# Optimization experiments

Hardware: AMD Instinct MI355X
Metric: run time of the kernel (lower is better)

Reference implementation:

```python
import jax, jax.numpy as jnp
import numpy as np

DIM = 1024
HEADS = 16
DIM_HEAD = 64
INNER = HEADS * DIM_HEAD
SCALE = DIM_HEAD ** -0.5


def rotate_half(t):
    # '... (j d) -> ... j d' with j=2: split last dim in half
    x1, x2 = jnp.split(t, 2, axis=-1)
    return jnp.concatenate((-x2, x1), axis=-1)


def rotary_pos(n, d, dtype):
    inv_freq = 1.0 / (10000.0 ** (jnp.arange(0, d, 2, dtype=jnp.float32) / d))
    freqs = jnp.arange(n, dtype=jnp.float32)[:, None] * inv_freq[None, :]  # (n, d/2)
    return jnp.concatenate((freqs, freqs), axis=-1).astype(dtype)  # (n, d)


def apply_rope(pos, t):
    return t * jnp.cos(pos) + rotate_half(t) * jnp.sin(pos)


def setup_inputs() -> dict:
    key = jax.random.key(0)
    ks = jax.random.split(key, 5)
    x = jax.random.normal(ks[0], (2, 2048, DIM), dtype=jnp.float32)
    gamma = jnp.ones((DIM,), dtype=jnp.float32)
    beta = jnp.zeros((DIM,), dtype=jnp.float32)
    Wq = jax.random.normal(ks[1], (DIM, INNER), dtype=jnp.float32) * 0.02
    Wkv = jax.random.normal(ks[2], (DIM, 2 * INNER), dtype=jnp.float32) * 0.02
    Wo = jax.random.normal(ks[3], (INNER, DIM), dtype=jnp.float32) * 0.02
    return {"x": x, "gamma": gamma, "beta": beta, "Wq": Wq, "Wkv": Wkv, "Wo": Wo}


def reference(x, gamma, beta, Wq, Wkv, Wo):
    b, n, _ = x.shape
    # LayerNorm with learned gamma, fixed-zero beta buffer
    mu = jnp.mean(x, axis=-1, keepdims=True)
    var = jnp.var(x, axis=-1, keepdims=True)
    xn = (x - mu) / jnp.sqrt(var + 1e-5) * gamma + beta

    q = xn @ Wq                       # (b, n, inner)
    kv = xn @ Wkv
    k, v = jnp.split(kv, 2, axis=-1)

    def to_heads(t):
        return t.reshape(b, n, HEADS, DIM_HEAD).transpose(0, 2, 1, 3)  # b h n d

    q, k, v = map(to_heads, (q, k, v))

    pos = rotary_pos(n, DIM_HEAD, x.dtype)  # (n, d)
    q = apply_rope(pos, q)
    k = apply_rope(pos, k)

    q = q * SCALE
    sim = jnp.einsum('bhid,bhjd->bhij', q, k)

    neg = -jnp.finfo(sim.dtype).max
    causal_mask = jnp.triu(jnp.ones((n, n), dtype=bool), k=1)
    sim = jnp.where(causal_mask, neg, sim)

    attn = jax.nn.softmax(sim, axis=-1)
    out = jnp.einsum('bhij,bhjd->bhid', attn, v)
    out = out.transpose(0, 2, 1, 3).reshape(b, n, INNER)
    return out @ Wo
```

## Files before the change

kernel.cpp:

```cpp
#include <hip/hip_runtime.h>
#include <stdint.h>

typedef unsigned short u16;
typedef __attribute__((ext_vector_type(8))) short short8;
typedef __attribute__((ext_vector_type(4))) float floatx4;
typedef __attribute__((ext_vector_type(4))) unsigned short u16x4;
typedef __attribute__((ext_vector_type(2))) unsigned int uint2v;

__device__ __forceinline__ float bf2f(u16 v) {
  union { uint32_t u; float f; } x; x.u = ((uint32_t)v) << 16; return x.f;
}
__device__ __forceinline__ u16 f2bf(float f) {
  union { float f; uint32_t u; } x; x.f = f;
  uint32_t r = x.u + 0x7fffu + ((x.u >> 16) & 1u);
  return (u16)(r >> 16);
}
__device__ __forceinline__ uint32_t fu(float f) {
  union { float f; uint32_t u; } x; x.f = f; return x.u;
}

#define GL2LDS(g, l)                                                          \
  __builtin_amdgcn_global_load_lds(                                           \
      (const __attribute__((address_space(1))) void*)(g),                     \
      (__attribute__((address_space(3))) void*)(l), 16, 0, 0)

#define WAITBAR(N)                                                            \
  asm volatile("s_waitcnt vmcnt(" #N ")\n\ts_barrier" ::: "memory")

__global__ __launch_bounds__(256) void prep_k(const float* __restrict__ x,
                                              const float* __restrict__ gamma,
                                              const float* __restrict__ beta,
                                              const float* __restrict__ Wq,
                                              const float* __restrict__ Wkv,
                                              const float* __restrict__ Wo,
                                              u16* __restrict__ xn,
                                              u16* __restrict__ wqkvT,
                                              u16* __restrict__ woT) {
  int bid = blockIdx.x;
  int t = threadIdx.x;
  if (bid < 4096) {
    int row = bid;
    const float* xr = x + (size_t)row * 1024;
    float4 xv = *(const float4*)(xr + t * 4);
    float v0 = xv.x, v1 = xv.y, v2 = xv.z, v3 = xv.w;
    float s = v0 + v1 + v2 + v3;
    float s2 = v0 * v0 + v1 * v1 + v2 * v2 + v3 * v3;
#pragma unroll
    for (int d = 1; d < 64; d <<= 1) {
      s += __shfl_xor(s, d, 64);
      s2 += __shfl_xor(s2, d, 64);
    }
    __shared__ float red[8];
    int lane = t & 63, wv = t >> 6;
    if (lane == 0) { red[wv] = s; red[4 + wv] = s2; }
    __syncthreads();
    s = red[0] + red[1] + red[2] + red[3];
    s2 = red[4] + red[5] + red[6] + red[7];
    float mu = s * (1.0f / 1024.0f);
    float var = s2 * (1.0f / 1024.0f) - mu * mu;
    float rstd = rsqrtf(var + 1e-5f);
    float4 gv = *(const float4*)(gamma + t * 4);
    float4 bv = *(const float4*)(beta + t * 4);
    u16x4 ov;
    ov.x = f2bf((v0 - mu) * rstd * gv.x + bv.x);
    ov.y = f2bf((v1 - mu) * rstd * gv.y + bv.y);
    ov.z = f2bf((v2 - mu) * rstd * gv.z + bv.z);
    ov.w = f2bf((v3 - mu) * rstd * gv.w + bv.w);
    *(u16x4*)(xn + (size_t)row * 1024 + t * 4) = ov;
  } else {
    __shared__ float tile[32][33];
    int wb = bid - 4096;
    const float* in;
    u16* outp;
    int C;
    if (wb < 1024) { in = Wq; outp = wqkvT; C = 1024; }
    else if (wb < 3072) { wb -= 1024; in = Wkv; outp = wqkvT + 1024 * 1024; C = 2048; }
    else { wb -= 3072; in = Wo; outp = woT; C = 1024; }
    int nbx = C >> 5;
    int c0 = (wb % nbx) * 32, r0 = (wb / nbx) * 32;
    int tx = t & 31, ty = t >> 5;
#pragma unroll
    for (int i = 0; i < 32; i += 8)
      tile[ty + i][tx] = in[(size_t)(r0 + ty + i) * C + c0 + tx];
    __syncthreads();
#pragma unroll
    for (int i = 0; i < 32; i += 8)
      outp[(size_t)(c0 + ty + i) * 1024 + r0 + tx] = f2bf(tile[tx][ty + i]);
  }
}

__global__ __launch_bounds__(256) void gemm_qkv_k(const u16* __restrict__ A,
                                                  const u16* __restrict__ BT,
                                                  u16* __restrict__ C) {
  const int K = 1024, lda = 1024, ldc = 3072;
  __shared__ __align__(16) u16 lA[3][128 * 32];
  __shared__ __align__(16) u16 lB[3][128 * 32];
  int tid = threadIdx.x;
  int bm = blockIdx.y * 128;
  int bn = blockIdx.x * 128;
  int w = tid >> 6, l = tid & 63;
  int wm = (w >> 1) * 64, wn = (w & 1) * 64;
  int lr = l & 15, lq = l >> 4;
  floatx4 acc[4][4] = {};
  int sr = w * 16 + (l >> 2);
  int sc = (l & 3) * 8;
  int sds = sr * 32 + sc;
  const u16* pA0 = A + (size_t)(bm + sr) * lda + sc;
  const u16* pA1 = pA0 + (size_t)64 * lda;
  const u16* pB0 = BT + (size_t)(bn + sr) * K + sc;
  const u16* pB1 = pB0 + (size_t)64 * K;
  int ao[4], bo[4];
#pragma unroll
  for (int i = 0; i < 4; i++) {
    ao[i] = (wm + i * 16 + lr) * 32 + lq * 8;
    bo[i] = (wn + i * 16 + lr) * 32 + lq * 8;
  }

#define STAGE_QKV(bi)                                                         \
  {                                                                           \
    GL2LDS(pA0, &lA[bi][sds]);                                                \
    GL2LDS(pA1, &lA[bi][sds + 2048]);                                         \
    GL2LDS(pB0, &lB[bi][sds]);                                                \
    GL2LDS(pB1, &lB[bi][sds + 2048]);                                         \
    pA0 += 32; pA1 += 32; pB0 += 32; pB1 += 32;                               \
  }
#define COMPUTE_QKV(bi)                                                       \
  {                                                                           \
    short8 afr[4], bfr[4];                                                    \
    _Pragma("unroll") for (int i = 0; i < 4; i++)                             \
        afr[i] = *(const short8*)(&lA[bi][ao[i]]);                            \
    _Pragma("unroll") for (int i = 0; i < 4; i++)                             \
        bfr[i] = *(const short8*)(&lB[bi][bo[i]]);                            \
    _Pragma("unroll") for (int mi = 0; mi < 4; mi++)                          \
        _Pragma("unroll") for (int ni = 0; ni < 4; ni++)                      \
            acc[mi][ni] = __builtin_amdgcn_mfma_f32_16x16x32_bf16(            \
                afr[mi], bfr[ni], acc[mi][ni], 0, 0, 0);                      \
  }

  STAGE_QKV(0);
  STAGE_QKV(1);
#pragma unroll 1
  for (int t = 0; t < 10; ++t) {
    WAITBAR(4); STAGE_QKV(2); COMPUTE_QKV(0);
    WAITBAR(4); STAGE_QKV(0); COMPUTE_QKV(1);
    WAITBAR(4); STAGE_QKV(1); COMPUTE_QKV(2);
  }
  WAITBAR(4); COMPUTE_QKV(0);
  WAITBAR(0); COMPUTE_QKV(1);

  int sec = bn >> 10;
  if (sec == 2) {
#pragma unroll
    for (int mi = 0; mi < 4; mi++)
#pragma unroll
      for (int ni = 0; ni < 4; ni++) {
        int col = bn + wn + ni * 16 + lr;
        int cv = col - 2048;
        int row = bm + wm + mi * 16 + lq * 4;
        int bq = row >> 11;
        int n = row & 2047;
        int bh = (bq << 4) | (cv >> 6);
        int d = cv & 63;
        size_t L = ((size_t)(bh * 64 + d) << 11) + n;
        u16x4 ov;
        ov.x = f2bf(acc[mi][ni][0]);
        ov.y = f2bf(acc[mi][ni][1]);
        ov.z = f2bf(acc[mi][ni][2]);
        ov.w = f2bf(acc[mi][ni][3]);
        *(u16x4*)(C + (L >> 10) * 3072 + 2048 + (L & 1023)) = ov;
      }
  } else {
    float QS = (sec == 0) ? 0.125f * 1.44269504088896f : 1.0f;
#pragma unroll
    for (int ni = 0; ni < 2; ni++) {
      int i = ni * 16 + lr;
      float invf = exp2f(-(float)i * 0.4152410118609203f);
#pragma unroll
      for (int mi = 0; mi < 4; mi++)
#pragma unroll
        for (int r = 0; r < 4; r++) {
          int row = bm + wm + mi * 16 + lq * 4 + r;
          int n = row & 2047;
          float ang = (float)n * invf;
          float s_, c_;
          __sincosf(ang, &s_, &c_);
          float x1 = acc[mi][ni][r], x2 = acc[mi][ni + 2][r];
          int col = bn + wn + ni * 16 + lr;
          C[(size_t)row * ldc + col] = f2bf((x1 * c_ - x2 * s_) * QS);
          C[(size_t)row * ldc + col + 32] = f2bf((x2 * c_ + x1 * s_) * QS);
        }
    }
  }
}

__global__ __launch_bounds__(256) void gemm64_bf16_k(const u16* __restrict__ A,
                                                     const u16* __restrict__ BT,
                                                     float* __restrict__ C,
                                                     int K, int lda, int ldc) {
  __shared__ __align__(16) u16 lA[3][64 * 32];
  __shared__ __align__(16) u16 lB[3][128 * 32];
  int tid = threadIdx.x;
  int bm = blockIdx.y * 64;
  int bn = blockIdx.x * 128;
  int w = tid >> 6, l = tid & 63;
  int wm = (w >> 1) * 32, wn = (w & 1) * 64;
  int lr = l & 15, lq = l >> 4;
  floatx4 acc[2][4] = {};
  int sr = w * 16 + (l >> 2);
  int sc = (l & 3) * 8;
  int sds = sr * 32 + sc;
  const u16* pA0 = A + (size_t)(bm + sr) * lda + sc;
  const u16* pB0 = BT + (size_t)(bn + sr) * K + sc;
  const u16* pB1 = pB0 + (size_t)64 * K;
  int ao[2], bo[4];
#pragma unroll
  for (int i = 0; i < 2; i++) ao[i] = (wm + i * 16 + lr) * 32 + lq * 8;
#pragma unroll
  for (int i = 0; i < 4; i++) bo[i] = (wn + i * 16 + lr) * 32 + lq * 8;

#define STAGE_O(bi)                                                           \
  {                                                                           \
    GL2LDS(pA0, &lA[bi][sds]);                                                \
    GL2LDS(pB0, &lB[bi][sds]);                                                \
    GL2LDS(pB1, &lB[bi][sds + 2048]);                                         \
    pA0 += 32; pB0 += 32; pB1 += 32;                                          \
  }
#define COMPUTE_O(bi)                                                         \
  {                                                                           \
    short8 afr[2], bfr[4];                                                    \
    _Pragma("unroll") for (int i = 0; i < 2; i++)                             \
        afr[i] = *(const short8*)(&lA[bi][ao[i]]);                            \
    _Pragma("unroll") for (int i = 0; i < 4; i++)                             \
        bfr[i] = *(const short8*)(&lB[bi][bo[i]]);                            \
    _Pragma("unroll") for (int mi = 0; mi < 2; mi++)                          \
        _Pragma("unroll") for (int ni = 0; ni < 4; ni++)                      \
            acc[mi][ni] = __builtin_amdgcn_mfma_f32_16x16x32_bf16(            \
                afr[mi], bfr[ni], acc[mi][ni], 0, 0, 0);                      \
  }

  STAGE_O(0);
  STAGE_O(1);
#pragma unroll 1
  for (int t = 0; t < 10; ++t) {
    WAITBAR(3); STAGE_O(2); COMPUTE_O(0);
    WAITBAR(3); STAGE_O(0); COMPUTE_O(1);
    WAITBAR(3); STAGE_O(1); COMPUTE_O(2);
  }
  WAITBAR(3); COMPUTE_O(0);
  WAITBAR(0); COMPUTE_O(1);

#pragma unroll
  for (int mi = 0; mi < 2; mi++)
#pragma unroll
    for (int ni = 0; ni < 4; ni++)
#pragma unroll
      for (int r = 0; r < 4; r++) {
        int row = bm + wm + mi * 16 + lq * 4 + r;
        int col = bn + wn + ni * 16 + lr;
        C[(size_t)row * ldc + col] = acc[mi][ni][r];
      }
}

#define LPT 64
#define FIXM 4.0f
__device__ __forceinline__ void attn_tile2(const u16* lK, const u16* lV, u16* lp,
                                           const short8* aq, floatx4* o,
                                           float& l_i, int lr, int lq,
                                           bool diag, int q0, int k0g,
                                           short8 ones) {
  floatx4 s[4];
#pragma unroll
  for (int ni = 0; ni < 4; ni++) {
    floatx4 a = {};
#pragma unroll
    for (int kc = 0; kc < 2; kc++) {
      int R = ni * 16 + lr;
      int c8 = (kc * 4 + lq) ^ (R & 7);
      short8 kf = *(const short8*)&lK[R * 64 + c8 * 8];
      a = __builtin_amdgcn_mfma_f32_16x16x32_bf16(kf, aq[kc], a, 0, 0, 0);
    }
    s[ni] = a;
  }
  if (diag) {
    int qg = q0 + lr;
#pragma unroll
    for (int ni = 0; ni < 4; ni++)
#pragma unroll
      for (int r = 0; r < 4; r++) {
        int kg = k0g + ni * 16 + lq * 4 + r;
        if (kg > qg) s[ni][r] = -1e30f;
      }
  }
  int swz = (lr & 7) << 3;
#pragma unroll
  for (int ni = 0; ni < 4; ni++) {
    float p0 = exp2f(s[ni][0] - FIXM), p1 = exp2f(s[ni][1] - FIXM);
    float p2 = exp2f(s[ni][2] - FIXM), p3 = exp2f(s[ni][3] - FIXM);
    uint2v dw;
    dw.x = __builtin_amdgcn_perm(fu(p1), fu(p0), 0x07060302u);
    dw.y = __builtin_amdgcn_perm(fu(p3), fu(p2), 0x07060302u);
    *(uint2v*)&lp[lr * LPT + ((ni * 16 + lq * 4) ^ swz)] = dw;
  }
  short8 pb0 = *(const short8*)&lp[lr * LPT + ((lq * 8) ^ swz)];
  short8 pb1 = *(const short8*)&lp[lr * LPT + ((32 + lq * 8) ^ swz)];
  floatx4 z = {};
  z = __builtin_amdgcn_mfma_f32_16x16x32_bf16(ones, pb0, z, 0, 0, 0);
  z = __builtin_amdgcn_mfma_f32_16x16x32_bf16(ones, pb1, z, 0, 0, 0);
  l_i += z[0];
#pragma unroll
  for (int di = 0; di < 4; di++) {
    int R = di * 16 + lr;
    int c80 = lq ^ (R & 7);
    int c81 = (4 + lq) ^ (R & 7);
    short8 v0 = *(const short8*)&lV[R * 64 + c80 * 8];
    o[di] = __builtin_amdgcn_mfma_f32_16x16x32_bf16(v0, pb0, o[di], 0, 0, 0);
    short8 v1 = *(const short8*)&lV[R * 64 + c81 * 8];
    o[di] = __builtin_amdgcn_mfma_f32_16x16x32_bf16(v1, pb1, o[di], 0, 0, 0);
  }
}

__global__ __launch_bounds__(256) void attn_k(const u16* __restrict__ qkv,
                                              u16* __restrict__ out) {
  __shared__ __align__(16) u16 lK[2][64 * 64];
  __shared__ __align__(16) u16 lV[2][64 * 64];
  __shared__ __align__(16) u16 lP[4][16 * LPT];
  int bh = blockIdx.x;
  int b = bh >> 4, h = bh & 15;
  int y = blockIdx.y;
  int g = y >> 3, o_ = y & 7;
  int j = (g & 1) ? ((g << 3) + 7 - o_) : y;
  int tid = threadIdx.x;
  int w = tid >> 6, l = tid & 63;
  int lr = l & 15, lq = l >> 4;
  int q0 = j * 64 + w * 16;
  const u16* qb = qkv + (size_t)b * 2048 * 3072 + h * 64;
  const u16* kb = qkv + (size_t)b * 2048 * 3072 + 1024 + h * 64;
  int bh64 = bh * 64;
  short8 aq[2];
  aq[0] = *(const short8*)(qb + (size_t)(q0 + lr) * 3072 + lq * 8);
  aq[1] = *(const short8*)(qb + (size_t)(q0 + lr) * 3072 + 32 + lq * 8);
  short8 ones;
#pragma unroll
  for (int i = 0; i < 8; i++) ones[i] = (short)0x3F80;
  floatx4 o[4] = {};
  float l_ = 0.0f;
  int srow8 = l >> 3;
  int sc8 = (l & 7) ^ srow8;
  u16* lp = &lP[w][0];
  auto stage = [&](int bufi, int kt) {
#pragma unroll
    for (int c = 0; c < 2; c++) {
      int m = w + c * 4;
      int row = m * 8 + srow8;
      GL2LDS(kb + (size_t)(kt * 64 + row) * 3072 + sc8 * 8, &lK[bufi][m * 512]);
      int nn = kt * 64 + sc8 * 8;
      GL2LDS(qkv + (size_t)((bh64 + row) * 2 + (nn >> 10)) * 3072 + 2048 +
                 (nn & 1023),
             &lV[bufi][m * 512]);
    }
  };
  stage(0, 0);
  for (int kt = 0; kt <= j; ++kt) {
    int cur = kt & 1;
    __syncthreads();
    if (kt < j) stage(cur ^ 1, kt + 1);
    attn_tile2(lK[cur], lV[cur], lp, aq, o, l_, lr, lq, kt == j, q0, kt * 64,
               ones);
  }
  float rl = 1.0f / l_;
#pragma unroll
  for (int di = 0; di < 4; di++) {
    uint2v dw;
    u16 a0 = f2bf(o[di][0] * rl), a1 = f2bf(o[di][1] * rl);
    u16 a2 = f2bf(o[di][2] * rl), a3 = f2bf(o[di][3] * rl);
    dw.x = (uint32_t)a0 | ((uint32_t)a1 << 16);
    dw.y = (uint32_t)a2 | ((uint32_t)a3 << 16);
    int dcol = h * 64 + di * 16 + lq * 4;
    *(uint2v*)(out + ((size_t)(b * 2048 + q0 + lr)) * 1024 + dcol) = dw;
  }
}

extern "C" void kernel_launch(void* const* d_in, const int* in_sizes, int n_in,
                              void* d_out, int out_size, void* d_ws, size_t ws_size,
                              hipStream_t stream) {
  const float* x = (const float*)d_in[0];
  const float* gamma = (const float*)d_in[1];
  const float* beta = (const float*)d_in[2];
  const float* Wq = (const float*)d_in[3];
  const float* Wkv = (const float*)d_in[4];
  const float* Wo = (const float*)d_in[5];
  float* out = (float*)d_out;
  char* ws = (char*)d_ws;

  u16* qkv = (u16*)(ws);
  u16* wqkvT = (u16*)(ws + 25165824);
  u16* woT = (u16*)(ws + 31457280);
  u16* xn = (u16*)(ws + 33554432);
  u16* attn_out = xn;

  prep_k<<<8192, 256, 0, stream>>>(x, gamma, beta, Wq, Wkv, Wo, xn, wqkvT, woT);
  gemm_qkv_k<<<dim3(24, 32), 256, 0, stream>>>(xn, wqkvT, qkv);
  attn_k<<<dim3(32, 32), 256, 0, stream>>>(qkv, attn_out);
  gemm64_bf16_k<<<dim3(8, 64), 256, 0, stream>>>(attn_out, woT, out, 1024, 1024, 1024);
}
```

Before: 196.1 us.

## Retile QKV GEMM to 256x256 blocks with 8 waves and swizzled LDS

Rewrites the QKV projection GEMM to use 256x256 output tiles with 512 threads (8 waves), a K-step of 64, and double-buffered LDS with an XOR swizzle to avoid bank conflicts. Global-to-LDS loads are interleaved with the MFMA phases, and s_setprio raises wave priority during matrix math. The aim is more reuse per loaded tile and better overlap of loads with compute. In exchange the grid shrinks to 192 blocks, which may underfill the GPU's compute units, and each thread holds twice as many accumulator registers.

```diff
diff --git a/kernel.cpp b/kernel.cpp
--- a/kernel.cpp
+++ b/kernel.cpp
@@ -26,6 +26,8 @@
 
 #define WAITBAR(N)                                                            \
   asm volatile("s_waitcnt vmcnt(" #N ")\n\ts_barrier" ::: "memory")
+#define BARX asm volatile("s_barrier" ::: "memory")
+#define VM0BARX asm volatile("s_waitcnt vmcnt(0)\n\ts_barrier" ::: "memory")
 
 __global__ __launch_bounds__(256) void prep_k(const float* __restrict__ x,
                                               const float* __restrict__ gamma,
@@ -89,84 +91,105 @@
   }
 }
 
-__global__ __launch_bounds__(256) void gemm_qkv_k(const u16* __restrict__ A,
-                                                  const u16* __restrict__ BT,
-                                                  u16* __restrict__ C) {
-  const int K = 1024, lda = 1024, ldc = 3072;
-  __shared__ __align__(16) u16 lA[3][128 * 32];
-  __shared__ __align__(16) u16 lB[3][128 * 32];
+__global__ __launch_bounds__(512, 2) void gemm_qkv_k(const u16* __restrict__ A,
+                                                     const u16* __restrict__ BT,
+                                                     u16* __restrict__ C) {
+  __shared__ __align__(16) u16 sA[2][16384];
+  __shared__ __align__(16) u16 sB[2][16384];
   int tid = threadIdx.x;
-  int bm = blockIdx.y * 128;
-  int bn = blockIdx.x * 128;
   int w = tid >> 6, l = tid & 63;
-  int wm = (w >> 1) * 64, wn = (w & 1) * 64;
   int lr = l & 15, lq = l >> 4;
-  floatx4 acc[4][4] = {};
-  int sr = w * 16 + (l >> 2);
-  int sc = (l & 3) * 8;
-  int sds = sr * 32 + sc;
-  const u16* pA0 = A + (size_t)(bm + sr) * lda + sc;
-  const u16* pA1 = pA0 + (size_t)64 * lda;
-  const u16* pB0 = BT + (size_t)(bn + sr) * K + sc;
-  const u16* pB1 = pB0 + (size_t)64 * K;
-  int ao[4], bo[4];
-#pragma unroll
-  for (int i = 0; i < 4; i++) {
-    ao[i] = (wm + i * 16 + lr) * 32 + lq * 8;
-    bo[i] = (wn + i * 16 + lr) * 32 + lq * 8;
-  }
-
-#define STAGE_QKV(bi)                                                         \
+  int wr = w >> 2, wc = w & 3;
+  int bm = blockIdx.y * 256;
+  int bn = blockIdx.x * 256;
+  floatx4 acc[8][4] = {};
+  int rl = w * 8 + (l >> 3);
+  int scol = ((l & 7) ^ ((l >> 3) & 7)) * 8;
+  int w512l8 = w * 512 + l * 8;
+  const u16* gA = A + (size_t)(bm + rl) * 1024 + scol;
+  const u16* gB = BT + (size_t)(bn + rl) * 1024 + scol;
+  int aab = wr * 8192 + lr * 64;
+  int bbb = (wc >> 1) * 8192 + ((wc & 1) * 64 + lr) * 64;
+  int cs0 = (lq * 8) ^ ((lr & 7) << 3);
+  int cs1 = (32 + lq * 8) ^ ((lr & 7) << 3);
+
+#define ST_A(bi)                                                              \
+  { GL2LDS(gA, &sA[bi][w512l8]);                                              \
+    GL2LDS(gA + 65536, &sA[bi][4096 + w512l8]);                               \
+    GL2LDS(gA + 131072, &sA[bi][8192 + w512l8]);                              \
+    GL2LDS(gA + 196608, &sA[bi][12288 + w512l8]); }
+#define ST_B0(bi)                                                             \
+  { GL2LDS(gB, &sB[bi][w512l8]);                                              \
+    GL2LDS(gB + 65536, &sB[bi][4096 + w512l8]); }
+#define ST_B1(bi)                                                             \
+  { GL2LDS(gB + 131072, &sB[bi][8192 + w512l8]);                              \
+    GL2LDS(gB + 196608, &sB[bi][12288 + w512l8]); }
+#define LDA4(bi, qm, cc)                                                      \
+  { af[0] = *(const short8*)&sA[bi][aab + (qm)*4096 + 0 + (cc)];              \
+    af[1] = *(const short8*)&sA[bi][aab + (qm)*4096 + 1024 + (cc)];           \
+    af[2] = *(const short8*)&sA[bi][aab + (qm)*4096 + 2048 + (cc)];           \
+    af[3] = *(const short8*)&sA[bi][aab + (qm)*4096 + 3072 + (cc)]; }
+#define LDB4(bi, cc)                                                          \
+  { bf[0] = *(const short8*)&sB[bi][bbb + 0 + (cc)];                          \
+    bf[1] = *(const short8*)&sB[bi][bbb + 1024 + (cc)];                       \
+    bf[2] = *(const short8*)&sB[bi][bbb + 2048 + (cc)];                       \
+    bf[3] = *(const short8*)&sB[bi][bbb + 3072 + (cc)]; }
+#define MM16(qm)                                                              \
+  _Pragma("unroll") for (int mi = 0; mi < 4; mi++)                            \
+  _Pragma("unroll") for (int ni = 0; ni < 4; ni++)                            \
+      acc[(qm)*4 + mi][ni] = __builtin_amdgcn_mfma_f32_16x16x32_bf16(         \
+          af[mi], bf[ni], acc[(qm)*4 + mi][ni], 0, 0, 0);
+#define KT(p, q, DOST)                                                        \
   {                                                                           \
-    GL2LDS(pA0, &lA[bi][sds]);                                                \
-    GL2LDS(pA1, &lA[bi][sds + 2048]);                                         \
-    GL2LDS(pB0, &lB[bi][sds]);                                                \
-    GL2LDS(pB1, &lB[bi][sds + 2048]);                                         \
-    pA0 += 32; pA1 += 32; pB0 += 32; pB1 += 32;                               \
-  }
-#define COMPUTE_QKV(bi)                                                       \
-  {                                                                           \
-    short8 afr[4], bfr[4];                                                    \
-    _Pragma("unroll") for (int i = 0; i < 4; i++)                             \
-        afr[i] = *(const short8*)(&lA[bi][ao[i]]);                            \
-    _Pragma("unroll") for (int i = 0; i < 4; i++)                             \
-        bfr[i] = *(const short8*)(&lB[bi][bo[i]]);                            \
-    _Pragma("unroll") for (int mi = 0; mi < 4; mi++)                          \
-        _Pragma("unroll") for (int ni = 0; ni < 4; ni++)                      \
-            acc[mi][ni] = __builtin_amdgcn_mfma_f32_16x16x32_bf16(            \
-                afr[mi], bfr[ni], acc[mi][ni], 0, 0, 0);                      \
-  }
-
-  STAGE_QKV(0);
-  STAGE_QKV(1);
+    short8 af[4], bf[4];                                                      \
+    LDA4(p, 0, cs0); LDB4(p, cs0);                                            \
+    if (DOST) ST_A(q);                                                        \
+    BARX; __builtin_amdgcn_s_setprio(1); MM16(0);                             \
+    __builtin_amdgcn_s_setprio(0); BARX;                                      \
+    LDA4(p, 1, cs0);                                                          \
+    if (DOST) ST_B0(q);                                                       \
+    BARX; __builtin_amdgcn_s_setprio(1); MM16(1);                             \
+    __builtin_amdgcn_s_setprio(0); BARX;                                      \
+    LDA4(p, 0, cs1); LDB4(p, cs1);                                            \
+    if (DOST) ST_B1(q);                                                       \
+    BARX; __builtin_amdgcn_s_setprio(1); MM16(0);                             \
+    __builtin_amdgcn_s_setprio(0); BARX;                                      \
+    LDA4(p, 1, cs1);                                                          \
+    if (DOST) { gA += 64; gB += 64; }                                         \
+    BARX; __builtin_amdgcn_s_setprio(1); MM16(1);                             \
+    __builtin_amdgcn_s_setprio(0); VM0BARX;                                   \
+  }
+
+  ST_A(0); ST_B0(0); ST_B1(0);
+  gA += 64; gB += 64;
+  VM0BARX;
 #pragma unroll 1
-  for (int t = 0; t < 10; ++t) {
-    WAITBAR(4); STAGE_QKV(2); COMPUTE_QKV(0);
-    WAITBAR(4); STAGE_QKV(0); COMPUTE_QKV(1);
-    WAITBAR(4); STAGE_QKV(1); COMPUTE_QKV(2);
-  }
-  WAITBAR(4); COMPUTE_QKV(0);
-  WAITBAR(0); COMPUTE_QKV(1);
+  for (int t = 0; t < 7; ++t) {
+    KT(0, 1, 1);
+    KT(1, 0, 1);
+  }
+  KT(0, 1, 1);
+  KT(1, 0, 0);
 
   int sec = bn >> 10;
   if (sec == 2) {
 #pragma unroll
-    for (int mi = 0; mi < 4; mi++)
+    for (int am = 0; am < 8; am++)
 #pragma unroll
       for (int ni = 0; ni < 4; ni++) {
-        int col = bn + wn + ni * 16 + lr;
+        int col = bn + wc * 64 + ni * 16 + lr;
         int cv = col - 2048;
-        int row = bm + wm + mi * 16 + lq * 4;
+        int row = bm + wr * 128 + (am >> 2) * 64 + (am & 3) * 16 + lq * 4;
         int bq = row >> 11;
         int n = row & 2047;
         int bh = (bq << 4) | (cv >> 6);
         int d = cv & 63;
         size_t L = ((size_t)(bh * 64 + d) << 11) + n;
         u16x4 ov;
-        ov.x = f2bf(acc[mi][ni][0]);
-        ov.y = f2bf(acc[mi][ni][1]);
-        ov.z = f2bf(acc[mi][ni][2]);
-        ov.w = f2bf(acc[mi][ni][3]);
+        ov.x = f2bf(acc[am][ni][0]);
+        ov.y = f2bf(acc[am][ni][1]);
+        ov.z = f2bf(acc[am][ni][2]);
+        ov.w = f2bf(acc[am][ni][3]);
         *(u16x4*)(C + (L >> 10) * 3072 + 2048 + (L & 1023)) = ov;
       }
   } else {
@@ -176,18 +199,18 @@
       int i = ni * 16 + lr;
       float invf = exp2f(-(float)i * 0.4152410118609203f);
 #pragma unroll
-      for (int mi = 0; mi < 4; mi++)
+      for (int am = 0; am < 8; am++)
 #pragma unroll
         for (int r = 0; r < 4; r++) {
-          int row = bm + wm + mi * 16 + lq * 4 + r;
+          int row = bm + wr * 128 + (am >> 2) * 64 + (am & 3) * 16 + lq * 4 + r;
           int n = row & 2047;
           float ang = (float)n * invf;
           float s_, c_;
           __sincosf(ang, &s_, &c_);
-          float x1 = acc[mi][ni][r], x2 = acc[mi][ni + 2][r];
-          int col = bn + wn + ni * 16 + lr;
-          C[(size_t)row * ldc + col] = f2bf((x1 * c_ - x2 * s_) * QS);
-          C[(size_t)row * ldc + col + 32] = f2bf((x2 * c_ + x1 * s_) * QS);
+          float x1 = acc[am][ni][r], x2 = acc[am][ni + 2][r];
+          int col = bn + wc * 64 + ni * 16 + lr;
+          C[(size_t)row * 3072 + col] = f2bf((x1 * c_ - x2 * s_) * QS);
+          C[(size_t)row * 3072 + col + 32] = f2bf((x2 * c_ + x1 * s_) * QS);
         }
     }
   }
@@ -399,7 +422,7 @@
   u16* attn_out = xn;
 
   prep_k<<<8192, 256, 0, stream>>>(x, gamma, beta, Wq, Wkv, Wo, xn, wqkvT, woT);
-  gemm_qkv_k<<<dim3(24, 32), 256, 0, stream>>>(xn, wqkvT, qkv);
+  gemm_qkv_k<<<dim3(12, 16), 512, 0, stream>>>(xn, wqkvT, qkv);
   attn_k<<<dim3(32, 32), 256, 0, stream>>>(qkv, attn_out);
   gemm64_bf16_k<<<dim3(8, 64), 256, 0, stream>>>(attn_out, woT, out, 1024, 1024, 1024);
 }
```

Result: faster. 192.2 us (-2.0%).
